# Performance work log

Hardware: AMD Instinct MI355X
Metric: run time of the kernel (lower is better)

## Reference

```python
import jax, jax.numpy as jnp
import numpy as np

B, T, D_MODEL, N_HEADS = 2, 2048, 2048, 16
HEAD_DIM = D_MODEL // N_HEADS
SCALE = HEAD_DIM ** -0.5
ROPE_THETA = 10000.0


def setup_inputs() -> dict:
    key = jax.random.key(0)
    ks = jax.random.split(key, 5)
    std = D_MODEL ** -0.5
    return {
        "x": jax.random.normal(ks[0], (B, T, D_MODEL), dtype=jnp.float32),
        "Wq": jax.random.normal(ks[1], (D_MODEL, D_MODEL), dtype=jnp.float32) * std,
        "Wk": jax.random.normal(ks[2], (D_MODEL, D_MODEL), dtype=jnp.float32) * std,
        "Wv": jax.random.normal(ks[3], (D_MODEL, D_MODEL), dtype=jnp.float32) * std,
        "Wo": jax.random.normal(ks[4], (D_MODEL, D_MODEL), dtype=jnp.float32) * std,
    }


def _rope_cos_sin(t, dtype):
    inv_freq = 1.0 / (ROPE_THETA ** (jnp.arange(0, HEAD_DIM, 2, dtype=jnp.float32) / HEAD_DIM))
    freqs = jnp.arange(t, dtype=jnp.float32)[:, None] * inv_freq[None, :]  # (T, hd/2)
    emb = jnp.concatenate([freqs, freqs], axis=-1)  # (T, hd)
    return jnp.cos(emb).astype(dtype), jnp.sin(emb).astype(dtype)


def _rotate_half(x):
    x1, x2 = jnp.split(x, 2, axis=-1)
    return jnp.concatenate([-x2, x1], axis=-1)


def _apply_rope(q, k):
    # q, k: (B, H, T, hd)
    cos, sin = _rope_cos_sin(q.shape[2], q.dtype)
    cos = cos[None, None]  # (1,1,T,hd)
    sin = sin[None, None]
    q = q * cos + _rotate_half(q) * sin
    k = k * cos + _rotate_half(k) * sin
    return q, k


def reference(x, Wq, Wk, Wv, Wo):
    b, t, _ = x.shape
    # projections (nn.Linear: x @ W.T), split heads: b t (h d) -> b h t d
    def proj(W):
        return jnp.einsum('btm,nm->btn', x, W).reshape(b, t, N_HEADS, HEAD_DIM).transpose(0, 2, 1, 3)
    Q, K, V = proj(Wq), proj(Wk), proj(Wv)
    Q, K = _apply_rope(Q, K)
    scores = jnp.einsum('bhtd,bhsd->bhts', Q, K) * SCALE  # (B,H,T,T)
    causal_mask = jnp.tril(jnp.ones((t, t), dtype=bool))
    scores = jnp.where(causal_mask[None, None], scores, -jnp.inf)
    attn = jax.nn.softmax(scores, axis=-1)
    attn = jnp.nan_to_num(attn, nan=0.0)
    out = jnp.einsum('bhts,bhsd->bhtd', attn, V)
    out = out.transpose(0, 2, 1, 3).reshape(b, t, D_MODEL)
    return jnp.einsum('btm,nm->btn', out, Wo)
```

## Files before the change

### kernel.cpp

```cpp
#include <hip/hip_runtime.h>

typedef unsigned short ushort_t;
typedef short bf16x8 __attribute__((ext_vector_type(8)));
typedef float f32x4 __attribute__((ext_vector_type(4)));

#define D_MODEL 2048
#define T_SEQ 2048
#define NB 2
#define NH 16
#define HD 128
#define M_ROWS 4096

__device__ __forceinline__ float b2f(unsigned short u) {
    return __uint_as_float(((unsigned)u) << 16);
}
__device__ __forceinline__ unsigned short f2b(float f) {
    unsigned u = __float_as_uint(f);
    u += 0x7fffu + ((u >> 16) & 1u);
    return (unsigned short)(u >> 16);
}

__device__ __forceinline__ void g2l16(const ushort_t* g, ushort_t* l) {
    __builtin_amdgcn_global_load_lds(
        (const __attribute__((address_space(1))) unsigned int*)g,
        (__attribute__((address_space(3))) unsigned int*)l, 16, 0, 0);
}

__global__ void detect_dtype(const ushort_t* __restrict__ x, int* __restrict__ flag) {
    __shared__ int cnt;
    if (threadIdx.x == 0) cnt = 0;
    __syncthreads();
    int c = 0;
    for (int i = threadIdx.x; i < 8192; i += 256) {
        int e = (x[i] >> 7) & 0xFF;
        if (e >= 0xC8) ++c;
    }
    atomicAdd(&cnt, c);
    __syncthreads();
    if (threadIdx.x == 0) *flag = (cnt > 16) ? 1 : 0;
}

__global__ void convert_all(const void* __restrict__ s0, const void* __restrict__ s1,
                            const void* __restrict__ s2, const void* __restrict__ s3,
                            const void* __restrict__ s4, ushort_t* __restrict__ dst,
                            const int* __restrict__ flag) {
    const size_t TENc = (size_t)M_ROWS * D_MODEL;
    const size_t WELc = (size_t)D_MODEL * D_MODEL;
    size_t i = ((size_t)blockIdx.x * 256 + threadIdx.x) * 8;
    const void* src;
    size_t off;
    if (i < TENc) {
        src = s0; off = i;
    } else {
        size_t j = i - TENc;
        int wsel = (int)(j >> 22);
        src = (wsel == 0) ? s1 : (wsel == 1) ? s2 : (wsel == 2) ? s3 : s4;
        off = j & (WELc - 1);
    }
    if (*flag) {
        const float* s = (const float*)src + off;
        union { ushort_t u[8]; float4 f; } pk;
        #pragma unroll
        for (int j2 = 0; j2 < 8; ++j2) pk.u[j2] = f2b(s[j2]);
        *(float4*)(dst + i) = pk.f;
    } else {
        *(float4*)(dst + i) = *(const float4*)((const ushort_t*)src + off);
    }
}

__global__ void rope_table(float* __restrict__ tab) {
    int tid = blockIdx.x * 256 + threadIdx.x;
    int i = tid & 63, t = tid >> 6;
    float ang = (float)t * exp2f(-(float)i * 0.20762050593046015f);
    tab[t * 128 + i]      = cosf(ang);
    tab[t * 128 + 64 + i] = sinf(ang);
}

#define SB2 (256 * 64)
#define SW2 (128 * 64)
#define SBUF2 (SB2 + SW2)

__global__ __launch_bounds__(512) void gemm_nt2(const ushort_t* __restrict__ A,
                                                const ushort_t* __restrict__ W,
                                                ushort_t* __restrict__ C,
                                                float* __restrict__ outf,
                                                const int* __restrict__ flag,
                                                const float* __restrict__ rtab,
                                                int mode, int Ndim) {
    __shared__ ushort_t smem[2 * SBUF2];
    const int tid  = threadIdx.x;
    const int lane = tid & 63;
    const int w    = tid >> 6;
    const int wr   = w >> 1;
    const int wc   = w & 1;
    const int quad = lane >> 4, l16 = lane & 15;
    const int Kd   = D_MODEL;

    const int wg  = blockIdx.y * 16 + blockIdx.x;
    const int swz = (wg & 7) * 32 + (wg >> 3);
    const long bm = (long)(swz >> 4) * 256;
    const long bn = (long)(swz & 15) * 128;

    int fl = *flag;
    asm volatile("" :: "v"(fl));
    asm volatile("s_waitcnt vmcnt(0)" ::: "memory");

    f32x4 acc[4][4];
    #pragma unroll
    for (int i = 0; i < 4; ++i)
        #pragma unroll
        for (int j = 0; j < 4; ++j) acc[i][j] = {0.f, 0.f, 0.f, 0.f};

    const int sw = l16 & 7;

    auto stage = [&](int kb, int buf) {
        ushort_t* As = smem + buf * SBUF2;
        ushort_t* Ws = As + SB2;
        #pragma unroll
        for (int i = 0; i < 4; ++i) {
            int ck = i * 512 + tid;
            int r = ck >> 3, g8 = (ck & 7) ^ (r & 7);
            g2l16(A + (bm + r) * Kd + kb + g8 * 8, As + (size_t)(i * 512 + w * 64) * 8);
        }
        #pragma unroll
        for (int i = 0; i < 2; ++i) {
            int ck = i * 512 + tid;
            int r = ck >> 3, g8 = (ck & 7) ^ (r & 7);
            g2l16(W + (bn + r) * Kd + kb + g8 * 8, Ws + (size_t)(i * 512 + w * 64) * 8);
        }
    };

    auto compute = [&](int buf) {
        const ushort_t* As = smem + buf * SBUF2;
        const ushort_t* Ws = As + SB2;
        #pragma unroll
        for (int kk2 = 0; kk2 < 2; ++kk2) {
            const int gb = kk2 * 4;
            bf16x8 af[4], bf[4];
            #pragma unroll
            for (int i = 0; i < 4; ++i)
                af[i] = *(const bf16x8*)(As + (wr * 64 + i * 16 + l16) * 64 + ((gb + quad) ^ sw) * 8);
            #pragma unroll
            for (int j = 0; j < 4; ++j)
                bf[j] = *(const bf16x8*)(Ws + (wc * 64 + j * 16 + l16) * 64 + ((gb + quad) ^ sw) * 8);
            #pragma unroll
            for (int i = 0; i < 4; ++i)
                #pragma unroll
                for (int j = 0; j < 4; ++j)
                    acc[i][j] = __builtin_amdgcn_mfma_f32_16x16x32_bf16(af[i], bf[j], acc[i][j], 0, 0, 0);
        }
    };

    stage(0, 0);
    stage(64, 1);
    for (int t = 0; t < 31; ++t) {
        asm volatile("s_waitcnt vmcnt(6)" ::: "memory");
        __builtin_amdgcn_sched_barrier(0);
        __builtin_amdgcn_s_barrier();
        __builtin_amdgcn_sched_barrier(0);
        compute(t & 1);
        asm volatile("s_waitcnt lgkmcnt(0)" ::: "memory");
        __builtin_amdgcn_sched_barrier(0);
        __builtin_amdgcn_s_barrier();
        __builtin_amdgcn_sched_barrier(0);
        if (t < 30) stage((t + 2) * 64, t & 1);
    }
    asm volatile("s_waitcnt vmcnt(0)" ::: "memory");
    __builtin_amdgcn_sched_barrier(0);
    __builtin_amdgcn_s_barrier();
    __builtin_amdgcn_sched_barrier(0);
    compute(1);
    __syncthreads();

    if (mode == 2) {
        #pragma unroll
        for (int i = 0; i < 4; ++i)
            #pragma unroll
            for (int j = 0; j < 4; ++j)
                #pragma unroll
                for (int r = 0; r < 4; ++r) {
                    int row = wr * 64 + i * 16 + quad * 4 + r;
                    int col = wc * 64 + j * 16 + l16;
                    smem[col * 256 + ((((row >> 3) ^ (col & 7)) << 3) | (row & 7))] =
                        f2b(acc[i][j][r]);
                }
        __syncthreads();
        const int b = (int)(bm >> 11), t0 = (int)(bm & 2047), h = (int)(bn >> 7);
        const size_t obase = ((size_t)(b * NH + h) * HD) * T_SEQ;
        #pragma unroll
        for (int it = 0; it < 8; ++it) {
            int dd  = it * 16 + (tid >> 5);
            int tch = tid & 31;
            bf16x8 v = *(const bf16x8*)(smem + dd * 256 + ((tch ^ (dd & 7)) << 3));
            *(bf16x8*)(C + obase + (size_t)dd * T_SEQ + t0 + tch * 8) = v;
        }
        return;
    }

    const int as_f32 = (outf != nullptr) && (fl != 0);
    if (!as_f32) {
        #pragma unroll
        for (int i = 0; i < 4; ++i)
            #pragma unroll
            for (int j = 0; j < 4; ++j)
                #pragma unroll
                for (int r = 0; r < 4; ++r) {
                    int row = wr * 64 + i * 16 + quad * 4 + r;
                    int col = wc * 64 + j * 16 + l16;
                    int ch = col >> 3, off = col & 7;
                    smem[row * 128 + (((ch ^ (row & 7)) << 3) | off)] = f2b(acc[i][j][r]);
                }
        __syncthreads();
        if (mode == 1) {
            #pragma unroll
            for (int it = 0; it < 8; ++it) {
                int row = it * 32 + (tid >> 4);
                int ch  = tid & 15;
                int t = (int)((bm + row) & 2047);
                bf16x8 v = *(const bf16x8*)(smem + row * 128 + ((ch ^ (row & 7)) << 3));
                bf16x8 p = *(const bf16x8*)(smem + row * 128 + (((ch ^ 8) ^ (row & 7)) << 3));
                const float* cr = rtab + t * 128 + (ch & 7) * 8;
                float sgn = (ch < 8) ? -1.f : 1.f;
                union { ushort_t u[8]; float4 f[1]; } o;
                #pragma unroll
                for (int j = 0; j < 8; ++j) {
                    float cv = cr[j], sv = cr[64 + j];
                    o.u[j] = f2b(b2f(((const ushort_t*)&v)[j]) * cv +
                                 sgn * b2f(((const ushort_t*)&p)[j]) * sv);
                }
                *(bf16x8*)(C + (bm + row) * Ndim + bn + ch * 8) = *(const bf16x8*)o.u;
            }
        } else {
            #pragma unroll
            for (int it = 0; it < 8; ++it) {
                int row = it * 32 + (tid >> 4);
                int ch  = tid & 15;
                bf16x8 v = *(const bf16x8*)(smem + row * 128 + ((ch ^ (row & 7)) << 3));
                *(bf16x8*)(C + (bm + row) * Ndim + bn + ch * 8) = v;
            }
        }
    } else {
        float* Fs = (float*)smem;
        #pragma unroll
        for (int half = 0; half < 2; ++half) {
            __syncthreads();
            if ((wr >> 1) == half) {
                #pragma unroll
                for (int i = 0; i < 4; ++i)
                    #pragma unroll
                    for (int j = 0; j < 4; ++j)
                        #pragma unroll
                        for (int r = 0; r < 4; ++r) {
                            int lr = (wr & 1) * 64 + i * 16 + quad * 4 + r;
                            int col = wc * 64 + j * 16 + l16;
                            int ch = col >> 2, off = col & 3;
                            Fs[lr * 128 + (((ch ^ (lr & 7)) << 2) | off)] = acc[i][j][r];
                        }
            }
            __syncthreads();
            #pragma unroll
            for (int it = 0; it < 8; ++it) {
                int lr = it * 16 + (tid >> 5);
                int ch = tid & 31;
                float4 v = *(const float4*)(Fs + lr * 128 + ((ch ^ (lr & 7)) << 2));
                *(float4*)(outf + (bm + half * 128 + lr) * Ndim + bn + ch * 4) = v;
            }
        }
    }
}

#define NQT (T_SEQ / 64)
#define C2SM 0.1275174452f
#define MFIX 96.0f

__global__ __launch_bounds__(256, 4) void attn_kernel(const ushort_t* __restrict__ Q,
                                                      const ushort_t* __restrict__ K,
                                                      const ushort_t* __restrict__ Vt,
                                                      ushort_t* __restrict__ O) {
    __shared__ ushort_t Ks[64 * 128];
    __shared__ ushort_t Vs[128 * 64];
    __shared__ ushort_t Ps[4 * 16 * 64];

    const int tid = threadIdx.x;
    const int lane = tid & 63, w = tid >> 6;
    const int quad = lane >> 4, l16 = lane & 15;
    const int bx = blockIdx.x;
    const int qb = (NQT - 1) - (bx >> 5);
    const int bh = bx & 31;
    const int h = bh & 15, b = bh >> 4;

    const size_t qkbase = ((size_t)(b * T_SEQ)) * D_MODEL + h * HD;
    const size_t vtbase = ((size_t)((b * NH + h) * HD)) * T_SEQ;
    const int ck0 = w * 256 + lane;
    ushort_t* Pw = Ps + w * 1024;

    auto stage_K = [&](int kvb) {
        #pragma unroll
        for (int i = 0; i < 4; ++i) {
            int ck = ck0 + i * 64;
            int r = ck >> 4, g = (ck & 15) ^ (r & 15);
            g2l16(K + qkbase + (size_t)(kvb * 64 + r) * D_MODEL + g * 8,
                  (ushort_t*)Ks + (size_t)(w * 256 + i * 64) * 8);
        }
    };
    auto stage_V = [&](int kvb) {
        #pragma unroll
        for (int i = 0; i < 4; ++i) {
            int ck = ck0 + i * 64;
            int r = ck >> 3, g = (ck & 7) ^ (r & 7);
            g2l16(Vt + vtbase + (size_t)r * T_SEQ + kvb * 64 + g * 8,
                  (ushort_t*)Vs + (size_t)(w * 256 + i * 64) * 8);
        }
    };

    bf16x8 qf[4];
    {
        const ushort_t* qrow = Q + qkbase + (size_t)(qb * 64 + w * 16 + l16) * D_MODEL;
        #pragma unroll
        for (int ks = 0; ks < 4; ++ks)
            qf[ks] = *(const bf16x8*)(qrow + ks * 32 + quad * 8);
    }

    float l_i[4] = {0.f, 0.f, 0.f, 0.f};
    f32x4 accO[8];
    for (int i = 0; i < 8; ++i) accO[i] = {0.f, 0.f, 0.f, 0.f};

    stage_K(0);

    for (int kvb = 0; kvb <= qb; ++kvb) {
        __syncthreads();
        stage_V(kvb);

        f32x4 accS[4];
        for (int i = 0; i < 4; ++i) accS[i] = {0.f, 0.f, 0.f, 0.f};
        __builtin_amdgcn_s_setprio(1);
        #pragma unroll
        for (int ks = 0; ks < 4; ++ks) {
            #pragma unroll
            for (int ct = 0; ct < 4; ++ct) {
                bf16x8 bb = *(const bf16x8*)(Ks + (ct * 16 + l16) * 128 +
                                             (((ks * 4 + quad) ^ l16) * 8));
                accS[ct] = __builtin_amdgcn_mfma_f32_16x16x32_bf16(qf[ks], bb, accS[ct], 0, 0, 0);
            }
        }
        __builtin_amdgcn_s_setprio(0);

        if (kvb == qb) {
            int qloc = w * 16 + quad * 4;
            for (int ct = 0; ct < 4; ++ct) {
                int key = ct * 16 + l16;
                for (int r = 0; r < 4; ++r)
                    if (key > qloc + r) accS[ct][r] = -1e30f;
            }
        }

        #pragma unroll
        for (int ct = 0; ct < 4; ++ct) {
            #pragma unroll
            for (int r = 0; r < 4; ++r) {
                float pv = exp2f((accS[ct][r] - MFIX) * C2SM);
                l_i[r] += pv;
                int col = ct * 16 + l16;
                int row = quad * 4 + r;
                Pw[row * 64 + ((((col >> 3) ^ (row & 7)) << 3) | (col & 7))] = f2b(pv);
            }
        }

        __syncthreads();
        if (kvb < qb) stage_K(kvb + 1);

        __builtin_amdgcn_s_setprio(1);
        #pragma unroll
        for (int kk2 = 0; kk2 < 2; ++kk2) {
            bf16x8 a = *(const bf16x8*)(Pw + l16 * 64 + (((kk2 * 4 + quad) ^ (l16 & 7)) << 3));
            #pragma unroll
            for (int ct = 0; ct < 8; ++ct) {
                bf16x8 bb = *(const bf16x8*)(Vs + (ct * 16 + l16) * 64 +
                                             (((kk2 * 4 + quad) ^ (l16 & 7)) * 8));
                accO[ct] = __builtin_amdgcn_mfma_f32_16x16x32_bf16(a, bb, accO[ct], 0, 0, 0);
            }
        }
        __builtin_amdgcn_s_setprio(0);
    }

    #pragma unroll
    for (int r = 0; r < 4; ++r) {
        for (int off = 1; off < 16; off <<= 1)
            l_i[r] += __shfl_xor(l_i[r], off);
        l_i[r] = 1.f / l_i[r];
    }

    for (int ct = 0; ct < 8; ++ct)
        for (int r = 0; r < 4; ++r) {
            size_t row = (size_t)(b * T_SEQ + qb * 64 + w * 16 + quad * 4 + r);
            O[row * D_MODEL + h * HD + ct * 16 + l16] = f2b(accO[ct][r] * l_i[r]);
        }
}

extern "C" void kernel_launch(void* const* d_in, const int* in_sizes, int n_in,
                              void* d_out, int out_size, void* d_ws, size_t ws_size,
                              hipStream_t stream) {
    const size_t TEN = (size_t)M_ROWS * D_MODEL;
    const size_t WEL = (size_t)D_MODEL * D_MODEL;

    char* ws = (char*)d_ws;
    int* flag = (int*)ws;
    ushort_t* xb  = (ushort_t*)(ws + 256);
    ushort_t* Wqb = xb  + TEN;
    ushort_t* Wkb = Wqb + WEL;
    ushort_t* Wvb = Wkb + WEL;
    ushort_t* Wob = Wvb + WEL;
    ushort_t* Qb  = Wob + WEL;
    ushort_t* Kb  = Qb + TEN;
    ushort_t* attn = Kb + TEN;
    ushort_t* Vt  = attn + TEN;
    float* rtab = (float*)(Vt + TEN);

    detect_dtype<<<1, 256, 0, stream>>>((const ushort_t*)d_in[0], flag);
    rope_table<<<(T_SEQ * 64) / 256, 256, 0, stream>>>(rtab);
    convert_all<<<(int)((TEN + 4 * WEL) / 8 / 256), 256, 0, stream>>>(
        d_in[0], d_in[1], d_in[2], d_in[3], d_in[4], xb, flag);

    dim3 gg(16, 16);
    gemm_nt2<<<gg, 512, 0, stream>>>(xb, Wqb, Qb, nullptr, flag, rtab, 1, D_MODEL);
    gemm_nt2<<<gg, 512, 0, stream>>>(xb, Wkb, Kb, nullptr, flag, rtab, 1, D_MODEL);
    gemm_nt2<<<gg, 512, 0, stream>>>(xb, Wvb, Vt, nullptr, flag, rtab, 2, D_MODEL);
    attn_kernel<<<dim3(NQT * NB * NH), 256, 0, stream>>>(Qb, Kb, Vt, attn);
    gemm_nt2<<<gg, 512, 0, stream>>>(attn, Wob, (ushort_t*)d_out, (float*)d_out, flag,
                                     rtab, 0, D_MODEL);
}
```

Measured before the change: 381.2 us.

## Rework GEMM into 4-stage K=32 pipeline with single barrier; reorder attention q-blocks

The GEMM main loop moves from a double-buffered K=64 tile with two barriers per step to a four-buffer ring of K=32 tiles. Loads are issued three steps ahead, each step has a single barrier, and s_setprio wraps the MFMA block. The aim is to hide global-to-LDS latency better and cut barrier stalls, at the cost of smaller compute chunks per sync and a new swizzle layout. Separately, the attention grid now interleaves long and short causal q-blocks rather than issuing them strictly longest-first, to balance load across CUs.

```diff
diff --git a/kernel.cpp b/kernel.cpp
--- a/kernel.cpp
+++ b/kernel.cpp
@@ -76,18 +76,18 @@
     tab[t * 128 + 64 + i] = sinf(ang);
 }
 
-#define SB2 (256 * 64)
-#define SW2 (128 * 64)
-#define SBUF2 (SB2 + SW2)
-
-__global__ __launch_bounds__(512) void gemm_nt2(const ushort_t* __restrict__ A,
+#define ABUF3 (256 * 32)
+#define WBUF3 (128 * 32)
+#define PBUF3 (ABUF3 + WBUF3)
+
+__global__ __launch_bounds__(512) void gemm_nt3(const ushort_t* __restrict__ A,
                                                 const ushort_t* __restrict__ W,
                                                 ushort_t* __restrict__ C,
                                                 float* __restrict__ outf,
                                                 const int* __restrict__ flag,
                                                 const float* __restrict__ rtab,
                                                 int mode, int Ndim) {
-    __shared__ ushort_t smem[2 * SBUF2];
+    __shared__ ushort_t smem[4 * PBUF3];
     const int tid  = threadIdx.x;
     const int lane = tid & 63;
     const int w    = tid >> 6;
@@ -111,65 +111,59 @@
         #pragma unroll
         for (int j = 0; j < 4; ++j) acc[i][j] = {0.f, 0.f, 0.f, 0.f};
 
-    const int sw = l16 & 7;
-
-    auto stage = [&](int kb, int buf) {
-        ushort_t* As = smem + buf * SBUF2;
-        ushort_t* Ws = As + SB2;
-        #pragma unroll
-        for (int i = 0; i < 4; ++i) {
-            int ck = i * 512 + tid;
-            int r = ck >> 3, g8 = (ck & 7) ^ (r & 7);
-            g2l16(A + (bm + r) * Kd + kb + g8 * 8, As + (size_t)(i * 512 + w * 64) * 8);
-        }
-        #pragma unroll
-        for (int i = 0; i < 2; ++i) {
-            int ck = i * 512 + tid;
-            int r = ck >> 3, g8 = (ck & 7) ^ (r & 7);
-            g2l16(W + (bn + r) * Kd + kb + g8 * 8, Ws + (size_t)(i * 512 + w * 64) * 8);
-        }
+    const int lr = lane >> 2;
+    const int cl = lane & 3;
+    const int rowA0 = (w * 2 + 0) * 16 + lr;
+    const int rowA1 = (w * 2 + 1) * 16 + lr;
+    const int rowW  = w * 16 + lr;
+    const ushort_t* gA0 = A + (bm + rowA0) * Kd + ((cl ^ ((rowA0 >> 1) & 3)) * 8);
+    const ushort_t* gA1 = A + (bm + rowA1) * Kd + ((cl ^ ((rowA1 >> 1) & 3)) * 8);
+    const ushort_t* gW  = W + (bn + rowW)  * Kd + ((cl ^ ((rowW  >> 1) & 3)) * 8);
+
+    const int fsl = (l16 >> 1) & 3;
+
+    auto stage = [&](int s) {
+        ushort_t* As = smem + (s & 3) * PBUF3;
+        ushort_t* Ws = As + ABUF3;
+        const int ko = s * 32;
+        g2l16(gA0 + ko, As + (w * 2 + 0) * 512);
+        g2l16(gA1 + ko, As + (w * 2 + 1) * 512);
+        g2l16(gW + ko, Ws + w * 512);
     };
 
-    auto compute = [&](int buf) {
-        const ushort_t* As = smem + buf * SBUF2;
-        const ushort_t* Ws = As + SB2;
-        #pragma unroll
-        for (int kk2 = 0; kk2 < 2; ++kk2) {
-            const int gb = kk2 * 4;
-            bf16x8 af[4], bf[4];
-            #pragma unroll
-            for (int i = 0; i < 4; ++i)
-                af[i] = *(const bf16x8*)(As + (wr * 64 + i * 16 + l16) * 64 + ((gb + quad) ^ sw) * 8);
-            #pragma unroll
-            for (int j = 0; j < 4; ++j)
-                bf[j] = *(const bf16x8*)(Ws + (wc * 64 + j * 16 + l16) * 64 + ((gb + quad) ^ sw) * 8);
-            #pragma unroll
-            for (int i = 0; i < 4; ++i)
-                #pragma unroll
-                for (int j = 0; j < 4; ++j)
-                    acc[i][j] = __builtin_amdgcn_mfma_f32_16x16x32_bf16(af[i], bf[j], acc[i][j], 0, 0, 0);
-        }
-    };
-
-    stage(0, 0);
-    stage(64, 1);
-    for (int t = 0; t < 31; ++t) {
-        asm volatile("s_waitcnt vmcnt(6)" ::: "memory");
+    auto kstep = [&](int s, int vm, bool do_stage) {
+        if (vm == 6)      asm volatile("s_waitcnt vmcnt(6)" ::: "memory");
+        else if (vm == 3) asm volatile("s_waitcnt vmcnt(3)" ::: "memory");
+        else              asm volatile("s_waitcnt vmcnt(0)" ::: "memory");
         __builtin_amdgcn_sched_barrier(0);
         __builtin_amdgcn_s_barrier();
         __builtin_amdgcn_sched_barrier(0);
-        compute(t & 1);
-        asm volatile("s_waitcnt lgkmcnt(0)" ::: "memory");
-        __builtin_amdgcn_sched_barrier(0);
-        __builtin_amdgcn_s_barrier();
-        __builtin_amdgcn_sched_barrier(0);
-        if (t < 30) stage((t + 2) * 64, t & 1);
-    }
-    asm volatile("s_waitcnt vmcnt(0)" ::: "memory");
-    __builtin_amdgcn_sched_barrier(0);
-    __builtin_amdgcn_s_barrier();
-    __builtin_amdgcn_sched_barrier(0);
-    compute(1);
+        if (do_stage) stage(s + 3);
+        const ushort_t* As = smem + (s & 3) * PBUF3;
+        const ushort_t* Ws = As + ABUF3;
+        bf16x8 af[4], bf[4];
+        #pragma unroll
+        for (int i = 0; i < 4; ++i)
+            af[i] = *(const bf16x8*)(As + (wr * 64 + i * 16 + l16) * 32 + (quad ^ fsl) * 8);
+        #pragma unroll
+        for (int j = 0; j < 4; ++j)
+            bf[j] = *(const bf16x8*)(Ws + (wc * 64 + j * 16 + l16) * 32 + (quad ^ fsl) * 8);
+        __builtin_amdgcn_s_setprio(1);
+        #pragma unroll
+        for (int i = 0; i < 4; ++i)
+            #pragma unroll
+            for (int j = 0; j < 4; ++j)
+                acc[i][j] = __builtin_amdgcn_mfma_f32_16x16x32_bf16(af[i], bf[j], acc[i][j], 0, 0, 0);
+        __builtin_amdgcn_s_setprio(0);
+    };
+
+    stage(0); stage(1); stage(2);
+    #pragma unroll 4
+    for (int s = 0; s < 60; ++s) kstep(s, 6, true);
+    kstep(60, 6, true);
+    kstep(61, 6, false);
+    kstep(62, 3, false);
+    kstep(63, 0, false);
     __syncthreads();
 
     if (mode == 2) {
@@ -251,19 +245,19 @@
                     for (int j = 0; j < 4; ++j)
                         #pragma unroll
                         for (int r = 0; r < 4; ++r) {
-                            int lr = (wr & 1) * 64 + i * 16 + quad * 4 + r;
+                            int lrow = (wr & 1) * 64 + i * 16 + quad * 4 + r;
                             int col = wc * 64 + j * 16 + l16;
                             int ch = col >> 2, off = col & 3;
-                            Fs[lr * 128 + (((ch ^ (lr & 7)) << 2) | off)] = acc[i][j][r];
+                            Fs[lrow * 128 + (((ch ^ (lrow & 7)) << 2) | off)] = acc[i][j][r];
                         }
             }
             __syncthreads();
             #pragma unroll
             for (int it = 0; it < 8; ++it) {
-                int lr = it * 16 + (tid >> 5);
+                int lrow = it * 16 + (tid >> 5);
                 int ch = tid & 31;
-                float4 v = *(const float4*)(Fs + lr * 128 + ((ch ^ (lr & 7)) << 2));
-                *(float4*)(outf + (bm + half * 128 + lr) * Ndim + bn + ch * 4) = v;
+                float4 v = *(const float4*)(Fs + lrow * 128 + ((ch ^ (lrow & 7)) << 2));
+                *(float4*)(outf + (bm + half * 128 + lrow) * Ndim + bn + ch * 4) = v;
             }
         }
     }
@@ -285,7 +279,12 @@
     const int lane = tid & 63, w = tid >> 6;
     const int quad = lane >> 4, l16 = lane & 15;
     const int bx = blockIdx.x;
-    const int qb = (NQT - 1) - (bx >> 5);
+    const int g = bx >> 5;
+    int qb;
+    if (g < 8)       qb = 31 - g;
+    else if (g < 16) qb = g - 8;
+    else if (g < 24) qb = 39 - g;
+    else             qb = g - 16;
     const int bh = bx & 31;
     const int h = bh & 15, b = bh >> 4;
 
@@ -298,8 +297,8 @@
         #pragma unroll
         for (int i = 0; i < 4; ++i) {
             int ck = ck0 + i * 64;
-            int r = ck >> 4, g = (ck & 15) ^ (r & 15);
-            g2l16(K + qkbase + (size_t)(kvb * 64 + r) * D_MODEL + g * 8,
+            int r = ck >> 4, gg = (ck & 15) ^ (r & 15);
+            g2l16(K + qkbase + (size_t)(kvb * 64 + r) * D_MODEL + gg * 8,
                   (ushort_t*)Ks + (size_t)(w * 256 + i * 64) * 8);
         }
     };
@@ -307,8 +306,8 @@
         #pragma unroll
         for (int i = 0; i < 4; ++i) {
             int ck = ck0 + i * 64;
-            int r = ck >> 3, g = (ck & 7) ^ (r & 7);
-            g2l16(Vt + vtbase + (size_t)r * T_SEQ + kvb * 64 + g * 8,
+            int r = ck >> 3, gg = (ck & 7) ^ (r & 7);
+            g2l16(Vt + vtbase + (size_t)r * T_SEQ + kvb * 64 + gg * 8,
                   (ushort_t*)Vs + (size_t)(w * 256 + i * 64) * 8);
         }
     };
@@ -422,10 +421,10 @@
         d_in[0], d_in[1], d_in[2], d_in[3], d_in[4], xb, flag);
 
     dim3 gg(16, 16);
-    gemm_nt2<<<gg, 512, 0, stream>>>(xb, Wqb, Qb, nullptr, flag, rtab, 1, D_MODEL);
-    gemm_nt2<<<gg, 512, 0, stream>>>(xb, Wkb, Kb, nullptr, flag, rtab, 1, D_MODEL);
-    gemm_nt2<<<gg, 512, 0, stream>>>(xb, Wvb, Vt, nullptr, flag, rtab, 2, D_MODEL);
+    gemm_nt3<<<gg, 512, 0, stream>>>(xb, Wqb, Qb, nullptr, flag, rtab, 1, D_MODEL);
+    gemm_nt3<<<gg, 512, 0, stream>>>(xb, Wkb, Kb, nullptr, flag, rtab, 1, D_MODEL);
+    gemm_nt3<<<gg, 512, 0, stream>>>(xb, Wvb, Vt, nullptr, flag, rtab, 2, D_MODEL);
     attn_kernel<<<dim3(NQT * NB * NH), 256, 0, stream>>>(Qb, Kb, Vt, attn);
-    gemm_nt2<<<gg, 512, 0, stream>>>(attn, Wob, (ushort_t*)d_out, (float*)d_out, flag,
+    gemm_nt3<<<gg, 512, 0, stream>>>(attn, Wob, (ushort_t*)d_out, (float*)d_out, flag,
                                      rtab, 0, D_MODEL);
 }
```

Result: no change. 377.3 us (-1.0%).
